# Kernel tuning notes

Hardware: AMD Instinct MI355X
Metric: run time of the kernel (lower is better)

## Reference

```python
import jax, jax.numpy as jnp
import numpy as np

ENC, DEC, B, S = 1024, 1024, 32, 2048


def setup_inputs() -> dict:
    key = jax.random.key(0)
    k1, k2, k3, k4, k5, k6 = jax.random.split(key, 6)
    scale_attn = 1.0 / np.sqrt(ENC + DEC)
    return {
        "decoder_hidden": jax.random.normal(k1, (B, DEC), dtype=jnp.float32),
        "encoder_outputs": jax.random.normal(k2, (B, S, ENC), dtype=jnp.float32),
        "mask": jax.random.randint(k3, (B, S), 0, 2, dtype=jnp.int32),
        "W_attn": jax.random.normal(k4, (ENC + DEC, DEC), dtype=jnp.float32) * scale_attn,
        "b_attn": jax.random.normal(k5, (DEC,), dtype=jnp.float32) * 0.02,
        "v_w": jax.random.normal(k6, (DEC,), dtype=jnp.float32) * (1.0 / np.sqrt(DEC)),
    }


def reference(decoder_hidden, encoder_outputs, mask, W_attn, b_attn, v_w):
    # Split cat((dec_exp, enc)) @ W into two GEMMs (same math, no repeat/concat).
    dec_dim = decoder_hidden.shape[-1]
    W_dec = W_attn[:dec_dim]      # [DEC, DEC]
    W_enc = W_attn[dec_dim:]      # [ENC, DEC]
    dec_proj = decoder_hidden @ W_dec                      # [B, DEC]
    enc_proj = jnp.einsum("bse,ed->bsd", encoder_outputs, W_enc)  # [B, S, DEC]
    energy = jnp.tanh(dec_proj[:, None, :] + enc_proj + b_attn)   # [B, S, DEC]
    scores = jnp.einsum("bsd,d->bs", energy, v_w)                 # [B, S]
    scores = jnp.where(mask == 0, -1e9, scores)
    attn_weights = jax.nn.softmax(scores, axis=1)                 # [B, S]
    context = jnp.einsum("bs,bse->be", attn_weights, encoder_outputs)  # [B, ENC]
    return (context, attn_weights)
```

## Files before the change

kernel.cpp:

```cpp
#include <hip/hip_runtime.h>
#include <hip/hip_bf16.h>
#include <cstdint>


#define ENCD 1024
#define DECD 1024
#define BATCH 32
#define SEQ 2048
#define MTOT (BATCH * SEQ)
#define KDIM 1024
#define NDIM 1024

typedef __attribute__((ext_vector_type(4))) float f32x4;
typedef __attribute__((ext_vector_type(8))) __bf16 bf16x8;
typedef __attribute__((ext_vector_type(8))) unsigned short u16x8;

__device__ __forceinline__ unsigned short f2bf(float f) {
  unsigned int u = __builtin_bit_cast(unsigned int, f);
  u += 0x7fffu + ((u >> 16) & 1u);
  return (unsigned short)(u >> 16);
}

__device__ __forceinline__ void async_lds16(const unsigned short* g, unsigned short* l) {
  __builtin_amdgcn_global_load_lds(
      (const __attribute__((address_space(1))) unsigned int*)g,
      (__attribute__((address_space(3))) unsigned int*)l, 16, 0, 0);
}

__global__ void conv_bf16_k(const float* __restrict__ src, unsigned short* __restrict__ dst) {
  const long i = ((long)blockIdx.x * 256 + threadIdx.x) * 8;
  const f32x4 f0 = *(const f32x4*)(src + i);
  const f32x4 f1 = *(const f32x4*)(src + i + 4);
  u16x8 v;
  v[0] = f2bf(f0[0]); v[1] = f2bf(f0[1]); v[2] = f2bf(f0[2]); v[3] = f2bf(f0[3]);
  v[4] = f2bf(f1[0]); v[5] = f2bf(f1[1]); v[6] = f2bf(f1[2]); v[7] = f2bf(f1[3]);
  *(u16x8*)(dst + i) = v;
}

__global__ void wt_k(const float* __restrict__ W, unsigned short* __restrict__ Wt) {
  __shared__ unsigned short t[64][65];
  const int k0 = blockIdx.x * 64, n0 = blockIdx.y * 64;
  const int tx = threadIdx.x & 63, ty = threadIdx.x >> 6;
#pragma unroll
  for (int i = 0; i < 16; ++i) {
    const int k = ty + i * 4;
    t[k][tx] = f2bf(W[(long)(DECD + k0 + k) * NDIM + n0 + tx]);
  }
  __syncthreads();
#pragma unroll
  for (int i = 0; i < 16; ++i) {
    const int n = ty + i * 4;
    Wt[(long)(n0 + n) * KDIM + k0 + tx] = t[tx][n];
  }
}

__global__ void dec_proj_k2(const float* __restrict__ dec, const float* __restrict__ W,
                            float* __restrict__ dp) {
  const int idx = blockIdx.x * 256 + threadIdx.x;
  const int kc = blockIdx.y;
  const int b = idx >> 10;
  const int n = idx & 1023;
  const float* d = dec + b * DECD + kc * 128;
  const float* w = W + (long)(kc * 128) * NDIM + n;
  float acc = 0.f;
#pragma unroll 8
  for (int k = 0; k < 128; ++k) acc = fmaf(d[k], w[(long)k * NDIM], acc);
  atomicAdd(&dp[idx], acc);
}

__global__ __launch_bounds__(256, 3) void gemm_scores_bf16(
    const unsigned short* __restrict__ Abf, const unsigned short* __restrict__ Wt,
    const float* __restrict__ dp, const float* __restrict__ bias,
    const float* __restrict__ vw, float* __restrict__ scores) {
  __shared__ unsigned short sA[128 * 64];
  __shared__ unsigned short sB[128 * 64];

  const int tid = threadIdx.x;
  const int lane = tid & 63;
  const int wave = tid >> 6;
  const int wm = wave >> 1, wn = wave & 1;
  const int quad = lane >> 4;
  const int l15 = lane & 15;

  const int bn = blockIdx.x;
  const int bm = blockIdx.y;
  const int n0 = bn * 128;
  const int row0 = bm * 128;
  const int bidx = bm >> 4;

  const int srow = lane >> 3;
  const int schunk = (lane & 7) ^ srow;

  const f32x4 zz = {0.f, 0.f, 0.f, 0.f};
  f32x4 acc[4][4];
#pragma unroll
  for (int i = 0; i < 4; ++i)
#pragma unroll
    for (int j = 0; j < 4; ++j) acc[i][j] = zz;

  for (int kt = 0; kt < 16; ++kt) {
    const int k0 = kt * 64;
    __syncthreads();
#pragma unroll
    for (int i = 0; i < 4; ++i) {
      const int r = wave * 32 + i * 8 + srow;
      async_lds16(Abf + (size_t)(row0 + r) * KDIM + k0 + schunk * 8,
                  &sA[(wave * 32 + i * 8) * 64]);
      async_lds16(Wt + (size_t)(n0 + r) * KDIM + k0 + schunk * 8,
                  &sB[(wave * 32 + i * 8) * 64]);
    }
    __syncthreads();
#pragma unroll
    for (int h = 0; h < 2; ++h) {
      bf16x8 af[4], bf[4];
      const int slot = ((h * 4 + quad) ^ (l15 & 7)) * 8;
#pragma unroll
      for (int t = 0; t < 4; ++t) {
        af[t] = __builtin_bit_cast(bf16x8, *(const u16x8*)&sA[(wm * 64 + t * 16 + l15) * 64 + slot]);
        bf[t] = __builtin_bit_cast(bf16x8, *(const u16x8*)&sB[(wn * 64 + t * 16 + l15) * 64 + slot]);
      }
#pragma unroll
      for (int mt = 0; mt < 4; ++mt)
#pragma unroll
        for (int nt = 0; nt < 4; ++nt)
          acc[mt][nt] = __builtin_amdgcn_mfma_f32_16x16x32_bf16(
              af[mt], bf[nt], acc[mt][nt], 0, 0, 0);
    }
  }

  float vv[4], dv[4];
#pragma unroll
  for (int nt = 0; nt < 4; ++nt) {
    const int n = n0 + wn * 64 + nt * 16 + l15;
    vv[nt] = vw[n];
    dv[nt] = dp[bidx * NDIM + n] + bias[n];
  }
#pragma unroll
  for (int mt = 0; mt < 4; ++mt) {
#pragma unroll
    for (int r = 0; r < 4; ++r) {
      float s = 0.f;
#pragma unroll
      for (int nt = 0; nt < 4; ++nt) {
        float x = acc[mt][nt][r] + dv[nt];
        x = fminf(fmaxf(x, -10.f), 10.f);
        const float e = __expf(2.f * x);
        s += (e - 1.f) * __builtin_amdgcn_rcpf(e + 1.f) * vv[nt];
      }
      s += __shfl_xor(s, 1);
      s += __shfl_xor(s, 2);
      s += __shfl_xor(s, 4);
      s += __shfl_xor(s, 8);
      if (l15 == 0) {
        const int m = row0 + wm * 64 + mt * 16 + quad * 4 + r;
        atomicAdd(&scores[m], s);
      }
    }
  }
}

__global__ __launch_bounds__(256, 2) void gemm_scores(
    const float* __restrict__ Ag, const unsigned short* __restrict__ Wt,
    const float* __restrict__ dp, const float* __restrict__ bias,
    const float* __restrict__ vw, float* __restrict__ scores) {
  __shared__ unsigned short sA[128 * 64];
  __shared__ unsigned short sB[128 * 64];
  const int tid = threadIdx.x;
  const int lane = tid & 63;
  const int wave = tid >> 6;
  const int wm = wave >> 1, wn = wave & 1;
  const int quad = lane >> 4;
  const int l15 = lane & 15;
  const int bn = blockIdx.x, bm = blockIdx.y;
  const int n0 = bn * 128, row0 = bm * 128, bidx = bm >> 4;
  const int sr = tid >> 3, sc = tid & 7;

  const f32x4 zz = {0.f, 0.f, 0.f, 0.f};
  f32x4 acc[4][4];
#pragma unroll
  for (int i = 0; i < 4; ++i)
#pragma unroll
    for (int j = 0; j < 4; ++j) acc[i][j] = zz;

  for (int kt = 0; kt < 16; ++kt) {
    const int k0 = kt * 64;
    __syncthreads();
#pragma unroll
    for (int j = 0; j < 4; ++j) {
      const int r = sr + 32 * j;
      const int c = sc ^ (r & 7);
      const float* src = Ag + (long)(row0 + r) * KDIM + (k0 + c * 8);
      f32x4 f0 = *(const f32x4*)src;
      f32x4 f1 = *(const f32x4*)(src + 4);
      u16x8 v;
      v[0] = f2bf(f0[0]); v[1] = f2bf(f0[1]); v[2] = f2bf(f0[2]); v[3] = f2bf(f0[3]);
      v[4] = f2bf(f1[0]); v[5] = f2bf(f1[1]); v[6] = f2bf(f1[2]); v[7] = f2bf(f1[3]);
      *(u16x8*)&sA[r * 64 + sc * 8] = v;
      const unsigned short* srcB = Wt + (long)(n0 + r) * KDIM + (k0 + c * 8);
      *(u16x8*)&sB[r * 64 + sc * 8] = *(const u16x8*)srcB;
    }
    __syncthreads();
#pragma unroll
    for (int h = 0; h < 2; ++h) {
      const int cs = ((h * 4 + quad) ^ (lane & 7)) * 8;
      bf16x8 af[4], bf[4];
#pragma unroll
      for (int t = 0; t < 4; ++t) {
        af[t] = __builtin_bit_cast(bf16x8, *(const u16x8*)&sA[(wm * 64 + t * 16 + l15) * 64 + cs]);
        bf[t] = __builtin_bit_cast(bf16x8, *(const u16x8*)&sB[(wn * 64 + t * 16 + l15) * 64 + cs]);
      }
#pragma unroll
      for (int mt = 0; mt < 4; ++mt)
#pragma unroll
        for (int nt = 0; nt < 4; ++nt)
          acc[mt][nt] = __builtin_amdgcn_mfma_f32_16x16x32_bf16(
              af[mt], bf[nt], acc[mt][nt], 0, 0, 0);
    }
  }

  float vv[4], dv[4];
#pragma unroll
  for (int nt = 0; nt < 4; ++nt) {
    const int n = n0 + wn * 64 + nt * 16 + l15;
    vv[nt] = vw[n];
    dv[nt] = dp[bidx * NDIM + n] + bias[n];
  }
#pragma unroll
  for (int mt = 0; mt < 4; ++mt) {
#pragma unroll
    for (int r = 0; r < 4; ++r) {
      float s = 0.f;
#pragma unroll
      for (int nt = 0; nt < 4; ++nt) {
        float x = acc[mt][nt][r] + dv[nt];
        x = fminf(fmaxf(x, -10.f), 10.f);
        const float e = __expf(2.f * x);
        s += (e - 1.f) * __builtin_amdgcn_rcpf(e + 1.f) * vv[nt];
      }
      s += __shfl_xor(s, 1);
      s += __shfl_xor(s, 2);
      s += __shfl_xor(s, 4);
      s += __shfl_xor(s, 8);
      if (l15 == 0) {
        const int m = row0 + wm * 64 + mt * 16 + quad * 4 + r;
        atomicAdd(&scores[m], s);
      }
    }
  }
}

__global__ void softmax_k(float* __restrict__ sc, const int* __restrict__ mask) {
  const int b = blockIdx.x;
  const int tid = threadIdx.x;
  const int w = tid >> 6;
  __shared__ float redm[4], reds[4];
  float* row = sc + b * SEQ;
  const int* mrow = mask + b * SEQ;
  float vals[8];
  float mx = -3.0e38f;
#pragma unroll
  for (int i = 0; i < 8; ++i) {
    const int s = tid + i * 256;
    float v = row[s];
    if (mrow[s] == 0) v = -1.0e9f;
    vals[i] = v;
    mx = fmaxf(mx, v);
  }
#pragma unroll
  for (int off = 1; off < 64; off <<= 1) mx = fmaxf(mx, __shfl_xor(mx, off));
  if ((tid & 63) == 0) redm[w] = mx;
  __syncthreads();
  mx = fmaxf(fmaxf(redm[0], redm[1]), fmaxf(redm[2], redm[3]));
  float sum = 0.f;
#pragma unroll
  for (int i = 0; i < 8; ++i) {
    vals[i] = __expf(vals[i] - mx);
    sum += vals[i];
  }
#pragma unroll
  for (int off = 1; off < 64; off <<= 1) sum += __shfl_xor(sum, off);
  if ((tid & 63) == 0) reds[w] = sum;
  __syncthreads();
  sum = reds[0] + reds[1] + reds[2] + reds[3];
  const float inv = 1.0f / sum;
#pragma unroll
  for (int i = 0; i < 8; ++i) row[tid + i * 256] = vals[i] * inv;
}

__global__ void context_k(const float* __restrict__ attn, const float* __restrict__ enc,
                          float* __restrict__ ctx) {
  const int b = blockIdx.y;
  const int s0 = blockIdx.x * 32;
  const int e = threadIdx.x * 4;
  const float* arow = attn + b * SEQ + s0;
  const float* ebase = enc + (long)(b * SEQ + s0) * ENCD + e;
  f32x4 acc = {0.f, 0.f, 0.f, 0.f};
#pragma unroll 8
  for (int s = 0; s < 32; ++s) {
    const float w = arow[s];
    const f32x4 v = *(const f32x4*)(ebase + (long)s * ENCD);
    acc += w * v;
  }
  float* dst = ctx + b * ENCD + e;
  atomicAdd(dst + 0, acc[0]);
  atomicAdd(dst + 1, acc[1]);
  atomicAdd(dst + 2, acc[2]);
  atomicAdd(dst + 3, acc[3]);
}

extern "C" void kernel_launch(void* const* d_in, const int* in_sizes, int n_in,
                              void* d_out, int out_size, void* d_ws, size_t ws_size,
                              hipStream_t stream) {
  (void)in_sizes; (void)n_in; (void)out_size;
  const float* dec  = (const float*)d_in[0];
  const float* enc  = (const float*)d_in[1];
  const int*   mask = (const int*)d_in[2];
  const float* W    = (const float*)d_in[3];
  const float* bias = (const float*)d_in[4];
  const float* vw   = (const float*)d_in[5];

  float* ctx    = (float*)d_out;
  float* scores = (float*)d_out + BATCH * ENCD;
  unsigned short* Wt  = (unsigned short*)d_ws;
  unsigned short* Abf = (unsigned short*)((char*)d_ws + (2u << 20));

  const bool fast = ws_size >= ((2ull << 20) + ((size_t)MTOT * KDIM * 2));

  hipMemsetAsync(scores, 0, (size_t)MTOT * sizeof(float), stream);
  hipMemsetAsync(ctx, 0, (size_t)(BATCH * NDIM) * sizeof(float), stream);
  wt_k<<<dim3(16, 16), 256, 0, stream>>>(W, Wt);
  dec_proj_k2<<<dim3(128, 8), 256, 0, stream>>>(dec, W, ctx);
  if (fast) {
    conv_bf16_k<<<32768, 256, 0, stream>>>(enc, Abf);
    gemm_scores_bf16<<<dim3(8, 512), 256, 0, stream>>>(Abf, Wt, ctx, bias, vw, scores);
  } else {
    gemm_scores<<<dim3(8, 512), 256, 0, stream>>>(enc, Wt, ctx, bias, vw, scores);
  }
  softmax_k<<<32, 256, 0, stream>>>(scores, mask);
  hipMemsetAsync(ctx, 0, (size_t)(BATCH * ENCD) * sizeof(float), stream);
  context_k<<<dim3(64, 32), 256, 0, stream>>>(scores, enc, ctx);
}
```

Measured before the change: 609.7 us.

## Replace atomics with partial-sum buffers and read bf16 encoder copy for context

New measurement: 569.2 us. -6.6%, faster.

```diff
diff --git a/kernel.cpp b/kernel.cpp
--- a/kernel.cpp
+++ b/kernel.cpp
@@ -19,6 +19,10 @@
   unsigned int u = __builtin_bit_cast(unsigned int, f);
   u += 0x7fffu + ((u >> 16) & 1u);
   return (unsigned short)(u >> 16);
+}
+
+__device__ __forceinline__ float bf2f(unsigned short h) {
+  return __builtin_bit_cast(float, (unsigned int)h << 16);
 }
 
 __device__ __forceinline__ void async_lds16(const unsigned short* g, unsigned short* l) {
@@ -52,6 +56,205 @@
     const int n = ty + i * 4;
     Wt[(long)(n0 + n) * KDIM + k0 + tx] = t[tx][n];
   }
+}
+
+__global__ void dec1_k(const float* __restrict__ dec, const float* __restrict__ W,
+                       float* __restrict__ part) {
+  const int idx = blockIdx.x * 256 + threadIdx.x;
+  const int kc = blockIdx.y;
+  const int b = idx >> 10;
+  const int n = idx & 1023;
+  const float* d = dec + b * DECD + kc * 128;
+  const float* w = W + (long)(kc * 128) * NDIM + n;
+  float acc = 0.f;
+#pragma unroll 8
+  for (int k = 0; k < 128; ++k) acc = fmaf(d[k], w[(long)k * NDIM], acc);
+  part[kc * 32768 + idx] = acc;
+}
+
+__global__ void dec2_k(const float* __restrict__ part, const float* __restrict__ bias,
+                       float* __restrict__ dp) {
+  const int idx = blockIdx.x * 256 + threadIdx.x;
+  float s = bias[idx & 1023];
+#pragma unroll
+  for (int kc = 0; kc < 8; ++kc) s += part[kc * 32768 + idx];
+  dp[idx] = s;
+}
+
+__global__ __launch_bounds__(256, 4) void gemm_fast(
+    const unsigned short* __restrict__ Abf, const unsigned short* __restrict__ Wt,
+    const float* __restrict__ dp, const float* __restrict__ vw,
+    float* __restrict__ sp) {
+  __shared__ unsigned short sA[128 * 64];
+  __shared__ unsigned short sB[128 * 64];
+
+  const int tid = threadIdx.x;
+  const int lane = tid & 63;
+  const int wave = tid >> 6;
+  const int wm = wave >> 1, wn = wave & 1;
+  const int quad = lane >> 4;
+  const int l15 = lane & 15;
+
+  const int bn = blockIdx.x;
+  const int bm = blockIdx.y;
+  const int n0 = bn * 128;
+  const int row0 = bm * 128;
+  const int bidx = bm >> 4;
+
+  const int srow = lane >> 3;
+  const int schunk = (lane & 7) ^ srow;
+
+  const f32x4 zz = {0.f, 0.f, 0.f, 0.f};
+  f32x4 acc[4][4];
+#pragma unroll
+  for (int i = 0; i < 4; ++i)
+#pragma unroll
+    for (int j = 0; j < 4; ++j) acc[i][j] = zz;
+
+  for (int kt = 0; kt < 16; ++kt) {
+    const int k0 = kt * 64;
+    __syncthreads();
+#pragma unroll
+    for (int i = 0; i < 4; ++i) {
+      const int r = wave * 32 + i * 8 + srow;
+      async_lds16(Abf + (size_t)(row0 + r) * KDIM + k0 + schunk * 8,
+                  &sA[(wave * 32 + i * 8) * 64]);
+      async_lds16(Wt + (size_t)(n0 + r) * KDIM + k0 + schunk * 8,
+                  &sB[(wave * 32 + i * 8) * 64]);
+    }
+    __syncthreads();
+#pragma unroll
+    for (int h = 0; h < 2; ++h) {
+      bf16x8 af[4], bf[4];
+      const int slot = ((h * 4 + quad) ^ (l15 & 7)) * 8;
+#pragma unroll
+      for (int t = 0; t < 4; ++t) {
+        af[t] = __builtin_bit_cast(bf16x8, *(const u16x8*)&sA[(wm * 64 + t * 16 + l15) * 64 + slot]);
+        bf[t] = __builtin_bit_cast(bf16x8, *(const u16x8*)&sB[(wn * 64 + t * 16 + l15) * 64 + slot]);
+      }
+#pragma unroll
+      for (int mt = 0; mt < 4; ++mt)
+#pragma unroll
+        for (int nt = 0; nt < 4; ++nt)
+          acc[mt][nt] = __builtin_amdgcn_mfma_f32_16x16x32_bf16(
+              af[mt], bf[nt], acc[mt][nt], 0, 0, 0);
+    }
+  }
+
+  float vv[4], dv[4];
+#pragma unroll
+  for (int nt = 0; nt < 4; ++nt) {
+    const int n = n0 + wn * 64 + nt * 16 + l15;
+    vv[nt] = vw[n];
+    dv[nt] = dp[bidx * NDIM + n];
+  }
+  float s_arr[4][4];
+#pragma unroll
+  for (int mt = 0; mt < 4; ++mt) {
+#pragma unroll
+    for (int r = 0; r < 4; ++r) {
+      float s = 0.f;
+#pragma unroll
+      for (int nt = 0; nt < 4; ++nt) {
+        float x = acc[mt][nt][r] + dv[nt];
+        x = fminf(fmaxf(x, -10.f), 10.f);
+        const float e = __expf(2.f * x);
+        s += (e - 1.f) * __builtin_amdgcn_rcpf(e + 1.f) * vv[nt];
+      }
+      s += __shfl_xor(s, 1);
+      s += __shfl_xor(s, 2);
+      s += __shfl_xor(s, 4);
+      s += __shfl_xor(s, 8);
+      s_arr[mt][r] = s;
+    }
+  }
+  __syncthreads();
+  float* sRed = (float*)sA;
+  if (wn == 1 && l15 == 0) {
+#pragma unroll
+    for (int mt = 0; mt < 4; ++mt)
+#pragma unroll
+      for (int r = 0; r < 4; ++r)
+        sRed[wm * 64 + mt * 16 + quad * 4 + r] = s_arr[mt][r];
+  }
+  __syncthreads();
+  if (wn == 0 && l15 == 0) {
+#pragma unroll
+    for (int mt = 0; mt < 4; ++mt)
+#pragma unroll
+      for (int r = 0; r < 4; ++r) {
+        const int ml = wm * 64 + mt * 16 + quad * 4 + r;
+        sp[(size_t)bn * MTOT + row0 + ml] = s_arr[mt][r] + sRed[ml];
+      }
+  }
+}
+
+__global__ void softmax_part_k(const float* __restrict__ sp, const int* __restrict__ mask,
+                               float* __restrict__ attn) {
+  const int b = blockIdx.x;
+  const int tid = threadIdx.x;
+  const int w = tid >> 6;
+  __shared__ float redm[4], reds[4];
+  const int* mrow = mask + b * SEQ;
+  float vals[8];
+  float mx = -3.0e38f;
+#pragma unroll
+  for (int i = 0; i < 8; ++i) {
+    const int s = tid + i * 256;
+    float v = 0.f;
+#pragma unroll
+    for (int bn = 0; bn < 8; ++bn) v += sp[(size_t)bn * MTOT + b * SEQ + s];
+    if (mrow[s] == 0) v = -1.0e9f;
+    vals[i] = v;
+    mx = fmaxf(mx, v);
+  }
+#pragma unroll
+  for (int off = 1; off < 64; off <<= 1) mx = fmaxf(mx, __shfl_xor(mx, off));
+  if ((tid & 63) == 0) redm[w] = mx;
+  __syncthreads();
+  mx = fmaxf(fmaxf(redm[0], redm[1]), fmaxf(redm[2], redm[3]));
+  float sum = 0.f;
+#pragma unroll
+  for (int i = 0; i < 8; ++i) {
+    vals[i] = __expf(vals[i] - mx);
+    sum += vals[i];
+  }
+#pragma unroll
+  for (int off = 1; off < 64; off <<= 1) sum += __shfl_xor(sum, off);
+  if ((tid & 63) == 0) reds[w] = sum;
+  __syncthreads();
+  sum = reds[0] + reds[1] + reds[2] + reds[3];
+  const float inv = 1.0f / sum;
+#pragma unroll
+  for (int i = 0; i < 8; ++i) attn[b * SEQ + tid + i * 256] = vals[i] * inv;
+}
+
+__global__ void ctx1_k(const float* __restrict__ attn, const unsigned short* __restrict__ Abf,
+                       float* __restrict__ part) {
+  const int sc = blockIdx.x;
+  const int b = blockIdx.y;
+  const int e0 = threadIdx.x * 8;
+  const float* arow = attn + b * SEQ + sc * 128;
+  const unsigned short* base = Abf + (size_t)(b * SEQ + sc * 128) * ENCD + e0;
+  float acc[8] = {0.f, 0.f, 0.f, 0.f, 0.f, 0.f, 0.f, 0.f};
+#pragma unroll 8
+  for (int s = 0; s < 128; ++s) {
+    const float w = arow[s];
+    const u16x8 v = *(const u16x8*)(base + (size_t)s * ENCD);
+#pragma unroll
+    for (int j = 0; j < 8; ++j) acc[j] = fmaf(w, bf2f(v[j]), acc[j]);
+  }
+  float* dst = part + (size_t)sc * (BATCH * ENCD) + b * ENCD + e0;
+  *(f32x4*)dst = *(f32x4*)&acc[0];
+  *(f32x4*)(dst + 4) = *(f32x4*)&acc[4];
+}
+
+__global__ void ctx2_k(const float* __restrict__ part, float* __restrict__ ctx) {
+  const int i = blockIdx.x * 256 + threadIdx.x;
+  float s = 0.f;
+#pragma unroll
+  for (int c = 0; c < 16; ++c) s += part[(size_t)c * (BATCH * ENCD) + i];
+  ctx[i] = s;
 }
 
 __global__ void dec_proj_k2(const float* __restrict__ dec, const float* __restrict__ W,
@@ -74,30 +277,22 @@
     const float* __restrict__ vw, float* __restrict__ scores) {
   __shared__ unsigned short sA[128 * 64];
   __shared__ unsigned short sB[128 * 64];
-
   const int tid = threadIdx.x;
   const int lane = tid & 63;
   const int wave = tid >> 6;
   const int wm = wave >> 1, wn = wave & 1;
   const int quad = lane >> 4;
   const int l15 = lane & 15;
-
-  const int bn = blockIdx.x;
-  const int bm = blockIdx.y;
-  const int n0 = bn * 128;
-  const int row0 = bm * 128;
-  const int bidx = bm >> 4;
-
+  const int bn = blockIdx.x, bm = blockIdx.y;
+  const int n0 = bn * 128, row0 = bm * 128, bidx = bm >> 4;
   const int srow = lane >> 3;
   const int schunk = (lane & 7) ^ srow;
-
   const f32x4 zz = {0.f, 0.f, 0.f, 0.f};
   f32x4 acc[4][4];
 #pragma unroll
   for (int i = 0; i < 4; ++i)
 #pragma unroll
     for (int j = 0; j < 4; ++j) acc[i][j] = zz;
-
   for (int kt = 0; kt < 16; ++kt) {
     const int k0 = kt * 64;
     __syncthreads();
@@ -127,7 +322,6 @@
               af[mt], bf[nt], acc[mt][nt], 0, 0, 0);
     }
   }
-
   float vv[4], dv[4];
 #pragma unroll
   for (int nt = 0; nt < 4; ++nt) {
@@ -151,15 +345,12 @@
       s += __shfl_xor(s, 2);
       s += __shfl_xor(s, 4);
       s += __shfl_xor(s, 8);
-      if (l15 == 0) {
-        const int m = row0 + wm * 64 + mt * 16 + quad * 4 + r;
-        atomicAdd(&scores[m], s);
-      }
-    }
-  }
-}
-
-__global__ __launch_bounds__(256, 2) void gemm_scores(
+      if (l15 == 0) atomicAdd(&scores[row0 + wm * 64 + mt * 16 + quad * 4 + r], s);
+    }
+  }
+}
+
+__global__ __launch_bounds__(256, 2) void gemm_scores_f32(
     const float* __restrict__ Ag, const unsigned short* __restrict__ Wt,
     const float* __restrict__ dp, const float* __restrict__ bias,
     const float* __restrict__ vw, float* __restrict__ scores) {
@@ -174,14 +365,12 @@
   const int bn = blockIdx.x, bm = blockIdx.y;
   const int n0 = bn * 128, row0 = bm * 128, bidx = bm >> 4;
   const int sr = tid >> 3, sc = tid & 7;
-
   const f32x4 zz = {0.f, 0.f, 0.f, 0.f};
   f32x4 acc[4][4];
 #pragma unroll
   for (int i = 0; i < 4; ++i)
 #pragma unroll
     for (int j = 0; j < 4; ++j) acc[i][j] = zz;
-
   for (int kt = 0; kt < 16; ++kt) {
     const int k0 = kt * 64;
     __syncthreads();
@@ -196,8 +385,7 @@
       v[0] = f2bf(f0[0]); v[1] = f2bf(f0[1]); v[2] = f2bf(f0[2]); v[3] = f2bf(f0[3]);
       v[4] = f2bf(f1[0]); v[5] = f2bf(f1[1]); v[6] = f2bf(f1[2]); v[7] = f2bf(f1[3]);
       *(u16x8*)&sA[r * 64 + sc * 8] = v;
-      const unsigned short* srcB = Wt + (long)(n0 + r) * KDIM + (k0 + c * 8);
-      *(u16x8*)&sB[r * 64 + sc * 8] = *(const u16x8*)srcB;
+      *(u16x8*)&sB[r * 64 + sc * 8] = *(const u16x8*)(Wt + (long)(n0 + r) * KDIM + (k0 + c * 8));
     }
     __syncthreads();
 #pragma unroll
@@ -217,7 +405,6 @@
               af[mt], bf[nt], acc[mt][nt], 0, 0, 0);
     }
   }
-
   float vv[4], dv[4];
 #pragma unroll
   for (int nt = 0; nt < 4; ++nt) {
@@ -241,10 +428,7 @@
       s += __shfl_xor(s, 2);
       s += __shfl_xor(s, 4);
       s += __shfl_xor(s, 8);
-      if (l15 == 0) {
-        const int m = row0 + wm * 64 + mt * 16 + quad * 4 + r;
-        atomicAdd(&scores[m], s);
-      }
+      if (l15 == 0) atomicAdd(&scores[row0 + wm * 64 + mt * 16 + quad * 4 + r], s);
     }
   }
 }
@@ -319,24 +503,40 @@
   const float* bias = (const float*)d_in[4];
   const float* vw   = (const float*)d_in[5];
 
-  float* ctx    = (float*)d_out;
-  float* scores = (float*)d_out + BATCH * ENCD;
+  float* ctx  = (float*)d_out;
+  float* attn = (float*)d_out + BATCH * ENCD;
   unsigned short* Wt  = (unsigned short*)d_ws;
-  unsigned short* Abf = (unsigned short*)((char*)d_ws + (2u << 20));
-
-  const bool fast = ws_size >= ((2ull << 20) + ((size_t)MTOT * KDIM * 2));
-
-  hipMemsetAsync(scores, 0, (size_t)MTOT * sizeof(float), stream);
-  hipMemsetAsync(ctx, 0, (size_t)(BATCH * NDIM) * sizeof(float), stream);
+  unsigned short* Abf = (unsigned short*)((char*)d_ws + (2ull << 20));
+  float* shared = (float*)((char*)d_ws + (130ull << 20));
+
+  const size_t needA = (132ull << 20);
+  const size_t needB = (2ull << 20) + ((size_t)MTOT * KDIM * 2);
+
   wt_k<<<dim3(16, 16), 256, 0, stream>>>(W, Wt);
-  dec_proj_k2<<<dim3(128, 8), 256, 0, stream>>>(dec, W, ctx);
-  if (fast) {
+  if (ws_size >= needA) {
+    dec1_k<<<dim3(128, 8), 256, 0, stream>>>(dec, W, shared);
+    dec2_k<<<128, 256, 0, stream>>>(shared, bias, ctx);
     conv_bf16_k<<<32768, 256, 0, stream>>>(enc, Abf);
-    gemm_scores_bf16<<<dim3(8, 512), 256, 0, stream>>>(Abf, Wt, ctx, bias, vw, scores);
+    gemm_fast<<<dim3(8, 512), 256, 0, stream>>>(Abf, Wt, ctx, vw, shared);
+    softmax_part_k<<<32, 256, 0, stream>>>(shared, mask, attn);
+    ctx1_k<<<dim3(16, 32), 128, 0, stream>>>(attn, Abf, shared);
+    ctx2_k<<<128, 256, 0, stream>>>(shared, ctx);
+  } else if (ws_size >= needB) {
+    hipMemsetAsync(attn, 0, (size_t)MTOT * sizeof(float), stream);
+    hipMemsetAsync(ctx, 0, (size_t)(BATCH * NDIM) * sizeof(float), stream);
+    dec_proj_k2<<<dim3(128, 8), 256, 0, stream>>>(dec, W, ctx);
+    conv_bf16_k<<<32768, 256, 0, stream>>>(enc, Abf);
+    gemm_scores_bf16<<<dim3(8, 512), 256, 0, stream>>>(Abf, Wt, ctx, bias, vw, attn);
+    softmax_k<<<32, 256, 0, stream>>>(attn, mask);
+    hipMemsetAsync(ctx, 0, (size_t)(BATCH * ENCD) * sizeof(float), stream);
+    context_k<<<dim3(64, 32), 256, 0, stream>>>(attn, enc, ctx);
   } else {
-    gemm_scores<<<dim3(8, 512), 256, 0, stream>>>(enc, Wt, ctx, bias, vw, scores);
-  }
-  softmax_k<<<32, 256, 0, stream>>>(scores, mask);
-  hipMemsetAsync(ctx, 0, (size_t)(BATCH * ENCD) * sizeof(float), stream);
-  context_k<<<dim3(64, 32), 256, 0, stream>>>(scores, enc, ctx);
-}
+    hipMemsetAsync(attn, 0, (size_t)MTOT * sizeof(float), stream);
+    hipMemsetAsync(ctx, 0, (size_t)(BATCH * NDIM) * sizeof(float), stream);
+    dec_proj_k2<<<dim3(128, 8), 256, 0, stream>>>(dec, W, ctx);
+    gemm_scores_f32<<<dim3(8, 512), 256, 0, stream>>>(enc, Wt, ctx, bias, vw, attn);
+    softmax_k<<<32, 256, 0, stream>>>(attn, mask);
+    hipMemsetAsync(ctx, 0, (size_t)(BATCH * ENCD) * sizeof(float), stream);
+    context_k<<<dim3(64, 32), 256, 0, stream>>>(attn, enc, ctx);
+  }
+}
```
